# Kernel tuning notes

Measured on AMD Instinct MI355X. Metric: run time of the kernel, lower is better.

The kernel has to match this reference:

```python
import jax, jax.numpy as jnp
import numpy as np

S = 32   # parent grid side
G = 64   # child grid side (2*S)
C = 16   # channels
DN = ('NDHWC', 'DHWIO', 'NDHWC')


def conv3(t, w, b):
    # t: [D,H,W,Cin] dense grid; zero padding == nonexistent coords contribute 0 (ME semantics)
    return jax.lax.conv_general_dilated(t[None], w, (1, 1, 1), 'SAME', dimension_numbers=DN)[0] + b


def _grids():
    ix = jnp.arange(G)
    px = (ix % 2)[:, None, None]
    py = (ix % 2)[None, :, None]
    pz = (ix % 2)[None, None, :]
    oct_m = {(a, b, c): (px == a) & (py == b) & (pz == c)
             for a in (0, 1) for b in (0, 1) for c in (0, 1)}
    groups6 = [[(0, 0, 0)], [(1, 1, 0)], [(1, 0, 1)], [(0, 1, 1)],
               [(1, 0, 0), (0, 1, 0)], [(0, 0, 1), (1, 1, 1)]]
    g6 = [jnp.any(jnp.stack([oct_m[o] for o in g]), 0) for g in groups6]
    s3 = (ix // 2)[:, None, None] + (ix // 2)[None, :, None] + (ix // 2)[None, None, :]
    m3 = [(s3 % 3) == j for j in range(3)]  # 3-way repartition (group_mask_gen_par)
    return g6, m3


def coder(feat, occ, w1, b1, w2, b2):
    # ProbCoder: conv -> ReLU -> conv -> sigmoid; outputs exist only at input coords
    of = occ[..., None].astype(feat.dtype)
    h = jax.nn.relu(conv3(feat, w1, b1)) * of
    return jax.nn.sigmoid(conv3(h, w2, b2)) * of


def union(a, b):
    (fa, oa), (fb, ob) = a, b
    return (jnp.where(oa[..., None], fa, fb), oa | ob)


def _forward(x, w_down, b_down, w_fel1, b_fel1, w_fel2, b_fel2, w_up, b_up,
             wc1, bc1, wc2, bc2, wl1, bl1, wl2, bl2):
    g6, m3 = _grids()
    occ_x = x[..., 0] > 0                                    # GT occupied child voxels
    # down (stride-2 conv): coordinate effect only -- last_POV uses ones_like features
    p_occ = jnp.any(occ_x.reshape(S, 2, S, 2, S, 2), axis=(1, 3, 5))  # parent coords
    pf = p_occ[..., None].astype(x.dtype)                    # last_POV features (ones)
    # FEL (dfa): conv(1->C,k3)+ReLU+conv(C->C,k3), outputs only at existing parents
    h = jax.nn.relu(conv3(pf, w_fel1, b_fel1)) * pf
    h = conv3(h, w_fel2, b_fel2) * pf                        # [S,S,S,C]
    # generative transposed conv k2 s2: each parent emits 8 children (octant-specific weight)
    up = jnp.einsum('xyzc,ocd->xyzod', h, w_up) + b_up       # [S,S,S,8,C]
    up = up.reshape(S, S, S, 2, 2, 2, C).transpose(0, 3, 1, 4, 2, 5, 6).reshape(G, G, G, C)
    occ = jnp.repeat(jnp.repeat(jnp.repeat(p_occ, 2, 0), 2, 1), 2, 2)  # child coords of prob
    prob_f = up * occ[..., None]
    lab = [occ_x & g for g in g6]                            # generate_label: GT per group
    # ---------- anchor1 compression (3 sub-stages inside octant group 1) ----------
    a1_o = occ & g6[0]
    a1_f = prob_f * a1_o[..., None]
    r = [(a1_f * m[..., None], a1_o & m) for m in m3]
    lab1 = [lab[0] & m for m in m3]
    p11 = coder(r[0][0], r[0][1], wc1[0], bc1[0], wc2[0], bc2[0])
    d1s = (prob_f * lab1[0][..., None], lab1[0])             # decoded GT of sub-stage 1
    in2 = union(r[1], d1s)
    p12 = coder(in2[0], in2[1], wl1[0], bl1[0], wl2[0], bl2[0]) * (in2[1] & m3[1])[..., None]
    d2s = (prob_f * lab1[1][..., None], lab1[1])
    in3 = union(union(d1s, d2s), r[2])
    p13 = coder(in3[0], in3[1], wl1[1], bl1[1], wl2[1], bl2[1]) * (in3[1] & m3[2])[..., None]
    # ---------- anchors 2..6 ----------
    dec = (prob_f * lab[0][..., None], lab[0])               # prob_anchor1_dec
    probs = [p11, p12, p13]
    for k in range(1, 6):
        ak_o = occ & g6[k]
        ak = (prob_f * ak_o[..., None], ak_o)
        inp = union(dec, ak)
        pk = coder(inp[0], inp[1], wc1[k], bc1[k], wc2[k], bc2[k]) * (inp[1] & g6[k])[..., None]
        probs.append(pk)
        if k < 5:
            dk = (prob_f * lab[k][..., None], lab[k])
            dec = union(dec, dk)
    probs = jnp.stack([p[..., 0] for p in probs], 0)          # [8,G,G,G]
    labels = jnp.stack([lab1[0], lab1[1], lab1[2], lab[1], lab[2], lab[3], lab[4], lab[5]], 0).astype(x.dtype)
    return probs, labels


def setup_inputs() -> dict:
    key = jax.random.key(0)
    ks = jax.random.split(key, 20)
    f = lambda k, s: jax.random.normal(k, s, jnp.float32) * 0.1
    x = (jax.random.uniform(ks[0], (G, G, G, 1)) < 0.5).astype(jnp.float32)
    return {
        'x': x,
        'w_down': f(ks[1], (2, 2, 2, 1, 1)), 'b_down': f(ks[2], (1,)),
        'w_fel1': f(ks[3], (3, 3, 3, 1, C)), 'b_fel1': f(ks[4], (C,)),
        'w_fel2': f(ks[5], (3, 3, 3, C, C)), 'b_fel2': f(ks[6], (C,)),
        'w_up': f(ks[7], (8, C, C)), 'b_up': f(ks[8], (C,)),
        'wc1': f(ks[9], (6, 3, 3, 3, C, C)), 'bc1': f(ks[10], (6, C)),
        'wc2': f(ks[11], (6, 3, 3, 3, C, 1)), 'bc2': f(ks[12], (6, 1)),
        'wl1': f(ks[13], (2, 5, 5, 5, C, C)), 'bl1': f(ks[14], (2, C)),
        'wl2': f(ks[15], (2, 5, 5, 5, C, 1)), 'bl2': f(ks[16], (2, 1)),
    }


def reference(x, w_down, b_down, w_fel1, b_fel1, w_fel2, b_fel2, w_up, b_up,
              wc1, bc1, wc2, bc2, wl1, bl1, wl2, bl2):
    return _forward(x, w_down, b_down, w_fel1, b_fel1, w_fel2, b_fel2, w_up, b_up,
                    wc1, bc1, wc2, bc2, wl1, bl1, wl2, bl2)
```

## Files before the change

kernel.cpp:

```cpp
#include <hip/hip_runtime.h>
#include <cstdint>
#include <math.h>

#define G 64
#define S 32
#define G3 (G*G*G)
#define S3 (S*S*S)

typedef unsigned long long u64;
typedef unsigned int u32;
typedef unsigned short u16;

typedef __attribute__((ext_vector_type(8))) short s16x8;
typedef __attribute__((ext_vector_type(4))) float f32x4;

__device__ __forceinline__ float sigmoidf_(float v) {
    return 1.0f / (1.0f + expf(-v));
}
__device__ __forceinline__ u32 f2bf_rne(float f) {
    u32 u = __float_as_uint(f);
    u += 0x7fff + ((u >> 16) & 1);
    return u >> 16;
}
__device__ __forceinline__ u64 rfl64(u64 v) {
    u32 lo = __builtin_amdgcn_readfirstlane((u32)v);
    u32 hi = __builtin_amdgcn_readfirstlane((u32)(v >> 32));
    return ((u64)hi << 32) | lo;
}
__device__ __forceinline__ u64 tap_hit(u64 wout, u64 wn, int dz) {
    return (dz >= 0) ? (wout & (wn >> dz)) : (wout & (wn << (-dz)));
}
__device__ __forceinline__ void gload16(const void* g, void* l) {
    __builtin_amdgcn_global_load_lds(
        (const __attribute__((address_space(1))) unsigned int*)g,
        (__attribute__((address_space(3))) unsigned int*)l, 16, 0, 0);
}

__global__ __launch_bounds__(256) void k_pocc(const float* __restrict__ x,
                                              unsigned char* __restrict__ pocc) {
    int p = blockIdx.x * 256 + threadIdx.x;
    if (p >= S3) return;
    int pz = p & 31, py = (p >> 5) & 31, px = p >> 10;
    const float* b = x + (((size_t)(px * 2) * G + py * 2) * G + pz * 2);
    bool occ = false;
    #pragma unroll
    for (int a = 0; a < 2; a++)
        #pragma unroll
        for (int bb = 0; bb < 2; bb++)
            #pragma unroll
            for (int c = 0; c < 2; c++)
                occ = occ || (b[((size_t)a * G + bb) * G + c] > 0.0f);
    pocc[p] = occ ? 1 : 0;
}

__global__ __launch_bounds__(256) void k_fel1(const unsigned char* __restrict__ pocc,
                                              const float* __restrict__ w1,
                                              const float* __restrict__ b1,
                                              float* __restrict__ h1) {
    int idx = blockIdx.x * 256 + threadIdx.x;
    int p = idx >> 4, co = idx & 15;
    int pz = p & 31, py = (p >> 5) & 31, px = p >> 10;
    if (!pocc[p]) { h1[idx] = 0.0f; return; }
    float a = b1[co];
    for (int dx = -1; dx <= 1; ++dx) {
        int nx = px + dx; if ((unsigned)nx >= S) continue;
        for (int dy = -1; dy <= 1; ++dy) {
            int ny = py + dy; if ((unsigned)ny >= S) continue;
            for (int dz = -1; dz <= 1; ++dz) {
                int nz = pz + dz; if ((unsigned)nz >= S) continue;
                if (pocc[(nx * S + ny) * S + nz])
                    a += w1[(((dx + 1) * 3 + (dy + 1)) * 3 + (dz + 1)) * 16 + co];
            }
        }
    }
    h1[idx] = fmaxf(a, 0.0f);
}

__global__ __launch_bounds__(256) void k_fel2(const unsigned char* __restrict__ pocc,
                                              const float* __restrict__ h1,
                                              const float* __restrict__ w2,
                                              const float* __restrict__ b2,
                                              float* __restrict__ h2) {
    int idx = blockIdx.x * 256 + threadIdx.x;
    int p = idx >> 4, co = idx & 15;
    int pz = p & 31, py = (p >> 5) & 31, px = p >> 10;
    if (!pocc[p]) { h2[idx] = 0.0f; return; }
    float a = b2[co];
    for (int dx = -1; dx <= 1; ++dx) {
        int nx = px + dx; if ((unsigned)nx >= S) continue;
        for (int dy = -1; dy <= 1; ++dy) {
            int ny = py + dy; if ((unsigned)ny >= S) continue;
            for (int dz = -1; dz <= 1; ++dz) {
                int nz = pz + dz; if ((unsigned)nz >= S) continue;
                const float* f = h1 + (size_t)((nx * S + ny) * S + nz) * 16;
                const float* ww = w2 + (size_t)(((dx + 1) * 3 + (dy + 1)) * 3 + (dz + 1)) * 256 + co;
                #pragma unroll
                for (int ci = 0; ci < 16; ++ci)
                    a = fmaf(f[ci], ww[ci * 16], a);
            }
        }
    }
    h2[idx] = a;
}

__global__ __launch_bounds__(256) void k_up(const unsigned char* __restrict__ pocc,
                                            const float* __restrict__ h2,
                                            const float* __restrict__ wup,
                                            const float* __restrict__ bup,
                                            u16* __restrict__ pf) {
    int idx = blockIdx.x * 256 + threadIdx.x;
    int p = idx >> 3, o = idx & 7;
    int pz = p & 31, py = (p >> 5) & 31, px = p >> 10;
    bool occ = pocc[p] != 0;
    int a = o >> 2, b = (o >> 1) & 1, c = o & 1;
    int line = (2 * px + a) * G + (2 * py + b);
    u16* op = pf + ((size_t)line * 64 + (2 * pz + c)) * 16;
    uint4* o4 = reinterpret_cast<uint4*>(op);
    if (!occ) {
        o4[0] = make_uint4(0, 0, 0, 0);
        o4[1] = make_uint4(0, 0, 0, 0);
        return;
    }
    float h[16];
    const float* hp = h2 + (size_t)p * 16;
    #pragma unroll
    for (int i = 0; i < 16; i++) h[i] = hp[i];
    u32 pk[8];
    #pragma unroll
    for (int i = 0; i < 8; ++i) {
        float a0 = bup[2 * i], a1 = bup[2 * i + 1];
        #pragma unroll
        for (int cc = 0; cc < 16; cc++) {
            a0 = fmaf(h[cc], wup[(o * 16 + cc) * 16 + 2 * i], a0);
            a1 = fmaf(h[cc], wup[(o * 16 + cc) * 16 + 2 * i + 1], a1);
        }
        pk[i] = f2bf_rne(a0) | (f2bf_rne(a1) << 16);
    }
    o4[0] = make_uint4(pk[0], pk[1], pk[2], pk[3]);
    o4[1] = make_uint4(pk[4], pk[5], pk[6], pk[7]);
}

__global__ __launch_bounds__(256) void k_masks(const float* __restrict__ x,
                                               const unsigned char* __restrict__ pocc,
                                               u64* __restrict__ lw_in,
                                               u64* __restrict__ lw_fin,
                                               float* __restrict__ labels) {
    int z = threadIdx.x;
    int y = blockIdx.x * 4 + threadIdx.y;
    int xx = blockIdx.y;
    int v = (xx * G + y) * G + z;
    int par = ((xx & 1) << 2) | ((y & 1) << 1) | (z & 1);
    const int gmap[8] = {0, 5, 4, 3, 4, 2, 1, 5};
    int g = gmap[par];
    int t = ((xx >> 1) + (y >> 1) + (z >> 1)) % 3;
    bool occ = pocc[(((xx >> 1) * S) + (y >> 1)) * S + (z >> 1)] != 0;
    bool ox = x[v] > 0.0f;
    bool g0 = (g == 0);

    bool mi[8], mf[8], lb[8];
    mi[0] = occ && g0 && (t == 0);
    mi[1] = (occ && g0 && (t == 1)) || (ox && g0 && (t == 0));
    mi[2] = (ox && g0 && (t < 2)) || (occ && g0 && (t == 2));
    mi[3] = (ox && g0)       || (occ && (g == 1));
    mi[4] = (ox && (g <= 1)) || (occ && (g == 2));
    mi[5] = (ox && (g <= 2)) || (occ && (g == 3));
    mi[6] = (ox && (g <= 3)) || (occ && (g == 4));
    mi[7] = (ox && (g <= 4)) || (occ && (g == 5));

    mf[0] = occ && g0 && (t == 0);
    mf[1] = occ && g0 && (t == 1);
    mf[2] = occ && g0 && (t == 2);
    mf[3] = occ && (g == 1);
    mf[4] = occ && (g == 2);
    mf[5] = occ && (g == 3);
    mf[6] = occ && (g == 4);
    mf[7] = occ && (g == 5);

    lb[0] = ox && g0 && (t == 0);
    lb[1] = ox && g0 && (t == 1);
    lb[2] = ox && g0 && (t == 2);
    lb[3] = ox && (g == 1);
    lb[4] = ox && (g == 2);
    lb[5] = ox && (g == 3);
    lb[6] = ox && (g == 4);
    lb[7] = ox && (g == 5);

    int line = xx * G + y;
    #pragma unroll
    for (int c = 0; c < 8; ++c) {
        u64 wi = __ballot((int)mi[c]);
        u64 wf = __ballot((int)mf[c]);
        if (z == 0) {
            lw_in[c * 4096 + line] = wi;
            lw_fin[c * 4096 + line] = wf;
        }
        labels[(size_t)c * G3 + v] = lb[c] ? 1.0f : 0.0f;
    }
}

#define FRAGSTRIDE 38400
__global__ __launch_bounds__(64) void k_prep_bfrag(const float* __restrict__ wc1,
                                                   const float* __restrict__ wl1,
                                                   u16* __restrict__ bfrag) {
    int c = blockIdx.x;
    int frag = blockIdx.y;
    int lane = threadIdx.x;
    bool is5 = (c == 1 || c == 2);
    int R = is5 ? 2 : 1;
    int KS = 2 * R + 1;
    int npair = R + 1;
    int nfrag = KS * KS * npair;
    if (frag >= nfrag) return;
    const float* W = is5 ? (wl1 + (size_t)(c - 1) * 32000)
                         : (wc1 + (size_t)((c == 0) ? 0 : (c - 2)) * 6912);
    int dxdy = frag / npair, p = frag - dxdy * npair;
    int dziA = 2 * p;
    int co = lane & 15, kg = lane >> 4;
    u16 outv[8];
    #pragma unroll
    for (int j = 0; j < 8; ++j) {
        int k = kg * 8 + j;
        int ci = k & 15;
        int dzi = (k < 16) ? dziA : (dziA + 1);
        float v = 0.0f;
        if (dzi < KS)
            v = W[(size_t)(dxdy * KS + dzi) * 256 + ci * 16 + co];
        outv[j] = (u16)f2bf_rne(v);
    }
    u16* o = bfrag + (size_t)c * FRAGSTRIDE + ((size_t)frag * 64 + lane) * 8;
    uint4 pk;
    pk.x = outv[0] | ((u32)outv[1] << 16);
    pk.y = outv[2] | ((u32)outv[3] << 16);
    pk.z = outv[4] | ((u32)outv[5] << 16);
    pk.w = outv[6] | ((u32)outv[7] << 16);
    *reinterpret_cast<uint4*>(o) = pk;
}

__global__ __launch_bounds__(256) void k_conv1_mfma(const u16* __restrict__ pf,
                                                    const u64* __restrict__ lw_in,
                                                    const u16* __restrict__ bfrag,
                                                    const float* __restrict__ bc1,
                                                    const float* __restrict__ bl1,
                                                    u16* __restrict__ hbase) {
    int c = blockIdx.y;
    bool is5 = (c == 1 || c == 2);
    int R = is5 ? 2 : 1;
    int KS = 2 * R + 1, npair = R + 1;
    const u64* lw = lw_in + (size_t)c * 4096;
    u16* h_c = hbase + (size_t)c * G3 * 16;
    const u16* bf = bfrag + (size_t)c * FRAGSTRIDE;
    const float* bptr = is5 ? (bl1 + (c - 1) * 16)
                            : (bc1 + ((c == 0) ? 0 : (c - 2)) * 16);

    int x = blockIdx.x >> 4;
    int y0 = (blockIdx.x & 15) << 2;
    int w = threadIdx.y;
    int lane = threadIdx.x;
    int yw = y0 + w;

    u64 w0 = rfl64(lw[x * G + yw]);
    u64 anyw = lw[x * G + y0] | lw[x * G + y0 + 1] | lw[x * G + y0 + 2] | lw[x * G + y0 + 3];
    if (anyw == 0ULL) return;

    __shared__ u32 lds[8 * 2304 / 4];
    char* ldsc = reinterpret_cast<char*>(lds);

    int col = lane & 15, kg = lane >> 4;
    float bv = bptr[col];
    f32x4 acc[4];
    #pragma unroll
    for (int s = 0; s < 4; ++s) acc[s] = (f32x4){bv, bv, bv, bv};

    int t = w * 64 + lane;
    if (t < 128) {
        int slot = t >> 4, q = t & 15;
        int off = (q < 8) ? (q * 16) : (2176 + (q - 8) * 16);
        *reinterpret_cast<uint4*>(ldsc + slot * 2304 + off) = make_uint4(0, 0, 0, 0);
    }

    u32 goff = ((u32)lane >> 1) * 32 +
               ((((u32)lane & 1) ^ (((u32)lane >> 3) & 1) ^ 1u) * 16);

    int nlines = 4 + 2 * R;

    for (int dx = -R; dx <= R; ++dx) {
        int nx = x + dx;
        __syncthreads();
        if ((unsigned)nx < G) {
            for (int s = w; s < nlines; s += 4) {
                int ny = y0 - R + s;
                u64 wn = ((unsigned)ny < G) ? lw[nx * G + ny] : 0ULL;
                if (wn != 0ULL) {
                    const char* src = reinterpret_cast<const char*>(
                        pf + (size_t)(nx * G + ny) * 1024) + goff;
                    char* dst = ldsc + s * 2304 + 128;
                    gload16(src, dst);
                    gload16(src + 1024, dst + 1024);
                }
            }
            asm volatile("s_waitcnt vmcnt(0)" ::: "memory");
            for (int s = w; s < nlines; s += 4) {
                int ny = y0 - R + s;
                u64 wn = ((unsigned)ny < G) ? lw[nx * G + ny] : 0ULL;
                bool live = (wn >> lane) & 1;
                if (!live) {
                    char* d = ldsc + s * 2304 + (lane + 4) * 32;
                    *reinterpret_cast<uint4*>(d) = make_uint4(0, 0, 0, 0);
                    *reinterpret_cast<uint4*>(d + 16) = make_uint4(0, 0, 0, 0);
                }
            }
        }
        __syncthreads();
        if (w0 == 0ULL || (unsigned)nx >= G) continue;

        for (int dy = -R; dy <= R; ++dy) {
            int ny = yw + dy;
            if ((unsigned)ny >= G) continue;
            u64 wn = rfl64(lw[nx * G + ny]);
            if (wn == 0ULL) continue;
            int slot = w + dy + R;
            for (int p = 0; p < npair; ++p) {
                int dzA = -R + 2 * p;
                int dzB = dzA + 1;
                bool hasB = (dzB <= R);
                u64 hit = tap_hit(w0, wn, dzA);
                if (hasB) hit |= tap_hit(w0, wn, dzB);
                if (hit == 0ULL) continue;
                int frag = ((dx + R) * KS + (dy + R)) * npair + p;
                s16x8 bf8 = *reinterpret_cast<const s16x8*>(bf + ((size_t)frag * 64 + lane) * 8);
                int dz = (kg < 2) ? dzA : (hasB ? dzB : dzA);
                int lzb = col + dz + 4;
                const char* ab = ldsc + slot * 2304 + lzb * 32
                                 + (((kg & 1) ^ ((lzb >> 2) & 1)) * 16);
                #pragma unroll
                for (int s = 0; s < 4; ++s) {
                    if (((hit >> (s * 16)) & 0xFFFFULL) == 0ULL) continue;
                    s16x8 a = *reinterpret_cast<const s16x8*>(ab + s * 512);
                    acc[s] = __builtin_amdgcn_mfma_f32_16x16x32_bf16(a, bf8, acc[s], 0, 0, 0);
                }
            }
        }
    }

    if (w0 == 0ULL) return;
    u16* hline = h_c + (size_t)(x * G + yw) * G * 16;
    #pragma unroll
    for (int s = 0; s < 4; ++s) {
        #pragma unroll
        for (int r = 0; r < 4; ++r) {
            int z = s * 16 + kg * 4 + r;
            if ((w0 >> z) & 1) {
                float v = fmaxf(acc[s][r], 0.0f);
                hline[z * 16 + col] = (u16)f2bf_rne(v);
            }
        }
    }
}

template <int KS>
__device__ __forceinline__ void conv2_body(const u32* __restrict__ h_c,
                                           const u64* __restrict__ lwi,
                                           const u64* __restrict__ lwf,
                                           const float* __restrict__ w2,
                                           const float* __restrict__ b2,
                                           float* __restrict__ outp) {
    const int R = KS / 2;
    int z = threadIdx.x;
    int line = blockIdx.x * 4 + threadIdx.y;
    int xx = line >> 6, y = line & 63;
    int v = (xx * G + y) * G + z;
    u64 wf = rfl64(lwf[line]);
    if (wf == 0ULL) { outp[v] = 0.0f; return; }
    bool m = (wf >> z) & 1;

    float ac0 = 0.0f, ac1 = 0.0f, ac2 = 0.0f, ac3 = 0.0f;
    for (int dx = -R; dx <= R; ++dx) {
        int nx = xx + dx; if ((unsigned)nx >= G) continue;
        for (int dy = -R; dy <= R; ++dy) {
            int ny = y + dy; if ((unsigned)ny >= G) continue;
            u64 wn = rfl64(lwi[nx * G + ny]);
            if (wn == 0ULL) continue;
            const float* wbase = w2 + (size_t)(((dx + R) * KS + (dy + R)) * KS) * 16;
            #pragma unroll
            for (int dz = -R; dz <= R; ++dz) {
                if (tap_hit(wf, wn, dz) == 0ULL) continue;
                int nz = z + dz;
                bool ok = (unsigned)nz < G;
                int nzc = ok ? nz : 0;
                bool mn = ok && ((wn >> nzc) & 1);
                const float* w = wbase + (dz + R) * 16;
                if (mn) {
                    const uint4* h4 = reinterpret_cast<const uint4*>(
                        h_c + ((size_t)((nx * G + ny) * G + nzc)) * 8);
                    uint4 Ua = h4[0], Ub = h4[1];
                    u32 uu[8] = {Ua.x, Ua.y, Ua.z, Ua.w, Ub.x, Ub.y, Ub.z, Ub.w};
                    float s0 = 0.0f, s1 = 0.0f;
                    #pragma unroll
                    for (int i = 0; i < 8; ++i) {
                        float lo = __uint_as_float(uu[i] << 16);
                        float hi = __uint_as_float(uu[i] & 0xffff0000u);
                        s0 = fmaf(lo, w[2 * i], s0);
                        s1 = fmaf(hi, w[2 * i + 1], s1);
                    }
                    const int sel = (dz + R) & 3;
                    if      (sel == 0) ac0 += s0 + s1;
                    else if (sel == 1) ac1 += s0 + s1;
                    else if (sel == 2) ac2 += s0 + s1;
                    else               ac3 += s0 + s1;
                }
            }
        }
    }
    float acc = b2[0] + ((ac0 + ac1) + (ac2 + ac3));
    outp[v] = m ? sigmoidf_(acc) : 0.0f;
}

__global__ __launch_bounds__(256) void k_conv2_all(const u32* __restrict__ hbase,
                                                   const u64* __restrict__ lw_in,
                                                   const u64* __restrict__ lw_fin,
                                                   const float* __restrict__ wc2,
                                                   const float* __restrict__ bc2,
                                                   const float* __restrict__ wl2,
                                                   const float* __restrict__ bl2,
                                                   float* __restrict__ out) {
    int c = blockIdx.y;
    const u64* lwi = lw_in + (size_t)c * 4096;
    const u64* lwf = lw_fin + (size_t)c * 4096;
    const u32* h_c = hbase + (size_t)c * G3 * 8;
    float* outp = out + (size_t)c * G3;
    if (c == 1 || c == 2) {
        conv2_body<5>(h_c, lwi, lwf, wl2 + (size_t)(c - 1) * 2000, bl2 + (c - 1), outp);
    } else {
        int j = (c == 0) ? 0 : (c - 2);
        conv2_body<3>(h_c, lwi, lwf, wc2 + (size_t)j * 432, bc2 + j, outp);
    }
}

extern "C" void kernel_launch(void* const* d_in, const int* in_sizes, int n_in,
                              void* d_out, int out_size, void* d_ws, size_t ws_size,
                              hipStream_t stream) {
    const float* x      = (const float*)d_in[0];
    const float* w_fel1 = (const float*)d_in[3];
    const float* b_fel1 = (const float*)d_in[4];
    const float* w_fel2 = (const float*)d_in[5];
    const float* b_fel2 = (const float*)d_in[6];
    const float* w_up   = (const float*)d_in[7];
    const float* b_up   = (const float*)d_in[8];
    const float* wc1    = (const float*)d_in[9];
    const float* bc1    = (const float*)d_in[10];
    const float* wc2    = (const float*)d_in[11];
    const float* bc2    = (const float*)d_in[12];
    const float* wl1    = (const float*)d_in[13];
    const float* bl1    = (const float*)d_in[14];
    const float* wl2    = (const float*)d_in[15];
    const float* bl2    = (const float*)d_in[16];
    float* out = (float*)d_out;

    char* ws = (char*)d_ws;
    u16*  probf16 = (u16*)(ws);
    float* h1     = (float*)(ws + 8388608);
    float* h2     = (float*)(ws + 10485760);
    unsigned char* pocc = (unsigned char*)(ws + 12582912);
    u64* lw_in  = (u64*)(ws + 12615680);
    u64* lw_fin = (u64*)(ws + 12877824);
    u16* bfrag  = (u16*)(ws + 13139968);
    u16* hbase  = (u16*)(ws + 13754368);

    k_pocc <<<dim3(S3 / 256), dim3(256), 0, stream>>>(x, pocc);
    k_fel1 <<<dim3(S3 * 16 / 256), dim3(256), 0, stream>>>(pocc, w_fel1, b_fel1, h1);
    k_fel2 <<<dim3(S3 * 16 / 256), dim3(256), 0, stream>>>(pocc, h1, w_fel2, b_fel2, h2);
    k_up   <<<dim3(S3 * 8 / 256), dim3(256), 0, stream>>>(pocc, h2, w_up, b_up, probf16);
    k_masks<<<dim3(16, 64), dim3(64, 4), 0, stream>>>(x, pocc, lw_in, lw_fin, out + (size_t)8 * G3);
    k_prep_bfrag<<<dim3(8, 75), dim3(64), 0, stream>>>(wc1, wl1, bfrag);

    k_conv1_mfma<<<dim3(1024, 8), dim3(64, 4), 0, stream>>>(
        probf16, lw_in, bfrag, bc1, bl1, hbase);
    k_conv2_all<<<dim3(1024, 8), dim3(64, 4), 0, stream>>>(
        (const u32*)hbase, lw_in, lw_fin, wc2, bc2, wl2, bl2, out);
}
```

Before: 210.9 us.

## Stage conv2 neighbour z-lines in LDS per x-slab for reuse across warps

The second coder conv now cooperatively loads the needed neighbouring y-lines of the bf16 hidden features into shared memory, one dx slice at a time, using async global-to-LDS copies with a swizzled layout. The four warps of a block then read their taps from LDS instead of issuing repeated global loads. This cuts redundant global and L2 traffic across the dy and dz taps. In exchange it adds two block barriers per dx and lets empty warps stay alive to help with loading.

```diff
diff --git a/kernel.cpp b/kernel.cpp
--- a/kernel.cpp
+++ b/kernel.cpp
@@ -357,50 +357,82 @@
     }
 }
 
-template <int KS>
-__device__ __forceinline__ void conv2_body(const u32* __restrict__ h_c,
-                                           const u64* __restrict__ lwi,
-                                           const u64* __restrict__ lwf,
-                                           const float* __restrict__ w2,
-                                           const float* __restrict__ b2,
-                                           float* __restrict__ outp) {
-    const int R = KS / 2;
-    int z = threadIdx.x;
-    int line = blockIdx.x * 4 + threadIdx.y;
-    int xx = line >> 6, y = line & 63;
-    int v = (xx * G + y) * G + z;
-    u64 wf = rfl64(lwf[line]);
-    if (wf == 0ULL) { outp[v] = 0.0f; return; }
-    bool m = (wf >> z) & 1;
+template <int R>
+__device__ __forceinline__ void conv2_lds_body(const u16* __restrict__ h16,
+                                               const u64* __restrict__ lwi,
+                                               const u64* __restrict__ lwf,
+                                               const float* __restrict__ w2,
+                                               const float* __restrict__ b2,
+                                               float* __restrict__ outp,
+                                               char* ldsc) {
+    const int KS = 2 * R + 1, NL = 4 + 2 * R;
+    int x = blockIdx.x >> 4;
+    int y0 = (blockIdx.x & 15) << 2;
+    int w = threadIdx.y;
+    int lane = threadIdx.x;
+    int yw = y0 + w;
+    int line = x * G + yw;
+    int v = line * G + lane;
+
+    u64 anyf = lwf[x * G + y0] | lwf[x * G + y0 + 1] |
+               lwf[x * G + y0 + 2] | lwf[x * G + y0 + 3];
+    if (anyf == 0ULL) { outp[v] = 0.0f; return; }
+    u64 wfv = rfl64(lwf[line]);
+    bool m = (wfv >> lane) & 1;
+
+    u32 goff = ((u32)lane >> 1) * 32 +
+               ((((u32)lane & 1) ^ (((u32)lane >> 3) & 1) ^ 1u) * 16);
 
     float ac0 = 0.0f, ac1 = 0.0f, ac2 = 0.0f, ac3 = 0.0f;
+
     for (int dx = -R; dx <= R; ++dx) {
-        int nx = xx + dx; if ((unsigned)nx >= G) continue;
+        int nx = x + dx;
+        __syncthreads();
+        if ((unsigned)nx < G) {
+            for (int s = w; s < NL; s += 4) {
+                int ny = y0 - R + s;
+                u64 wn = ((unsigned)ny < G) ? lwi[nx * G + ny] : 0ULL;
+                if (wn != 0ULL) {
+                    const char* src = reinterpret_cast<const char*>(
+                        h16 + (size_t)(nx * G + ny) * 1024) + goff;
+                    char* dst = ldsc + s * 2304 + 128;
+                    gload16(src, dst);
+                    gload16(src + 1024, dst + 1024);
+                }
+            }
+        }
+        __syncthreads();
+        if (wfv == 0ULL || (unsigned)nx >= G) continue;
+
         for (int dy = -R; dy <= R; ++dy) {
-            int ny = y + dy; if ((unsigned)ny >= G) continue;
+            int ny = yw + dy;
+            if ((unsigned)ny >= G) continue;
             u64 wn = rfl64(lwi[nx * G + ny]);
             if (wn == 0ULL) continue;
+            const char* sb = ldsc + (w + dy + R) * 2304;
             const float* wbase = w2 + (size_t)(((dx + R) * KS + (dy + R)) * KS) * 16;
             #pragma unroll
             for (int dz = -R; dz <= R; ++dz) {
-                if (tap_hit(wf, wn, dz) == 0ULL) continue;
-                int nz = z + dz;
+                if (tap_hit(wfv, wn, dz) == 0ULL) continue;
+                int nz = lane + dz;
                 bool ok = (unsigned)nz < G;
                 int nzc = ok ? nz : 0;
                 bool mn = ok && ((wn >> nzc) & 1);
-                const float* w = wbase + (dz + R) * 16;
+                const float* wt = wbase + (dz + R) * 16;
                 if (mn) {
-                    const uint4* h4 = reinterpret_cast<const uint4*>(
-                        h_c + ((size_t)((nx * G + ny) * G + nzc)) * 8);
-                    uint4 Ua = h4[0], Ub = h4[1];
+                    int lzb = nzc + 4;
+                    int sw = ((lzb >> 2) & 1) * 16;
+                    const char* ab = sb + lzb * 32;
+                    uint4 Ua = *reinterpret_cast<const uint4*>(ab + sw);
+                    uint4 Ub = *reinterpret_cast<const uint4*>(ab + (16 - sw));
                     u32 uu[8] = {Ua.x, Ua.y, Ua.z, Ua.w, Ub.x, Ub.y, Ub.z, Ub.w};
                     float s0 = 0.0f, s1 = 0.0f;
                     #pragma unroll
                     for (int i = 0; i < 8; ++i) {
                         float lo = __uint_as_float(uu[i] << 16);
                         float hi = __uint_as_float(uu[i] & 0xffff0000u);
-                        s0 = fmaf(lo, w[2 * i], s0);
-                        s1 = fmaf(hi, w[2 * i + 1], s1);
+                        s0 = fmaf(lo, wt[2 * i], s0);
+                        s1 = fmaf(hi, wt[2 * i + 1], s1);
                     }
                     const int sel = (dz + R) & 3;
                     if      (sel == 0) ac0 += s0 + s1;
@@ -415,7 +447,7 @@
     outp[v] = m ? sigmoidf_(acc) : 0.0f;
 }
 
-__global__ __launch_bounds__(256) void k_conv2_all(const u32* __restrict__ hbase,
+__global__ __launch_bounds__(256) void k_conv2_all(const u16* __restrict__ hbase,
                                                    const u64* __restrict__ lw_in,
                                                    const u64* __restrict__ lw_fin,
                                                    const float* __restrict__ wc2,
@@ -423,16 +455,17 @@
                                                    const float* __restrict__ wl2,
                                                    const float* __restrict__ bl2,
                                                    float* __restrict__ out) {
+    __shared__ char lds[8 * 2304];
     int c = blockIdx.y;
     const u64* lwi = lw_in + (size_t)c * 4096;
     const u64* lwf = lw_fin + (size_t)c * 4096;
-    const u32* h_c = hbase + (size_t)c * G3 * 8;
+    const u16* h_c = hbase + (size_t)c * G3 * 16;
     float* outp = out + (size_t)c * G3;
     if (c == 1 || c == 2) {
-        conv2_body<5>(h_c, lwi, lwf, wl2 + (size_t)(c - 1) * 2000, bl2 + (c - 1), outp);
+        conv2_lds_body<2>(h_c, lwi, lwf, wl2 + (size_t)(c - 1) * 2000, bl2 + (c - 1), outp, lds);
     } else {
         int j = (c == 0) ? 0 : (c - 2);
-        conv2_body<3>(h_c, lwi, lwf, wc2 + (size_t)j * 432, bc2 + j, outp);
+        conv2_lds_body<1>(h_c, lwi, lwf, wc2 + (size_t)j * 432, bc2 + j, outp, lds);
     }
 }
 
@@ -476,5 +509,5 @@
     k_conv1_mfma<<<dim3(1024, 8), dim3(64, 4), 0, stream>>>(
         probf16, lw_in, bfrag, bc1, bl1, hbase);
     k_conv2_all<<<dim3(1024, 8), dim3(64, 4), 0, stream>>>(
-        (const u32*)hbase, lw_in, lw_fin, wc2, bc2, wl2, bl2, out);
-}
+        hbase, lw_in, lw_fin, wc2, bc2, wl2, bl2, out);
+}
```

Result: slower. 222.0 us (+5.2%).
